# Kernel optimization log

Hardware: AMD Instinct MI355X
Metric: run time of the kernel (lower is better)

## Reference

```python
import jax, jax.numpy as jnp
import numpy as np

N_NODES = 80000
N_EDGES = 1280000
IN_C, HID_C, OUT_C = 128, 64, 40


def setup_inputs() -> dict:
    key = jax.random.key(0)
    k1, k2, k3, k4 = jax.random.split(key, 4)
    x = jax.random.normal(k1, (N_NODES, IN_C), dtype=jnp.float32)
    edge_index = jax.random.randint(k2, (2, N_EDGES), 0, N_NODES, dtype=jnp.int32)
    W1 = jax.random.normal(k3, (IN_C, HID_C), dtype=jnp.float32) * (1.0 / np.sqrt(IN_C))
    W2 = jax.random.normal(k4, (HID_C, OUT_C), dtype=jnp.float32) * (1.0 / np.sqrt(HID_C))
    return {"x": x, "edge_index": edge_index, "W1": W1, "W2": W2}


def _spmm_add(edge_index, h):
    # adj_t.matmul(h): out[dst] += h[src]  (aggr='add', message = x_j)
    src, dst = edge_index[0], edge_index[1]
    return jax.ops.segment_sum(h[src], dst, num_segments=N_NODES)


def reference(x, edge_index, W1, W2):
    # GCNConv 1: linear (no bias) then add-aggregate SpMM
    h = _spmm_add(edge_index, x @ W1)          # [N, HID]
    h = jax.nn.relu(h)
    # GCNConv 2
    h = _spmm_add(edge_index, h @ W2)          # [N, OUT]
    return jax.nn.log_softmax(h, axis=-1)
```

## Files before the change

kernel.cpp:

```cpp
#include <hip/hip_runtime.h>
#include <hip/hip_bf16.h>
#include <math.h>

#define N_NODES 80000
#define N_EDGES 1280000
#define IN_C 128
#define HID_C 64
#define OUT_C 40

#define KB 313
#define BK_CAP 4600
#define EPT_A 8

__device__ __forceinline__ float bf_lo(unsigned u) {
    union { unsigned i; float f; } c; c.i = u << 16; return c.f;
}
__device__ __forceinline__ float bf_hi(unsigned u) {
    union { unsigned i; float f; } c; c.i = u & 0xffff0000u; return c.f;
}
__device__ __forceinline__ unsigned pack_bf2(float a, float b) {
    union { float f; unsigned i; } ca, cb; ca.f = a; cb.f = b;
    unsigned ra = (ca.i + 0x7fffu + ((ca.i >> 16) & 1u)) >> 16;
    unsigned rb = (cb.i + 0x7fffu + ((cb.i >> 16) & 1u)) >> 16;
    return ra | (rb << 16);
}

typedef short v8s __attribute__((ext_vector_type(8)));
typedef float v4f __attribute__((ext_vector_type(4)));
typedef float v2f __attribute__((ext_vector_type(2)));
union U16 { uint4 u; v8s s; };

__device__ __forceinline__ v2f bf2f(unsigned u) {
    return (v2f){bf_lo(u), bf_hi(u)};
}

__global__ void prep_w_kernel(const float* __restrict__ W1, const float* __restrict__ W2,
                              unsigned* __restrict__ w1t, unsigned* __restrict__ w2t,
                              int* __restrict__ bcnt) {
    const int g = blockIdx.x * 256 + threadIdx.x;
    if (g < KB) bcnt[g] = 0;
    {
        const int wcol = g >> 6, kk = g & 63;
        w1t[g] = pack_bf2(W1[(2 * kk) * HID_C + wcol], W1[(2 * kk + 1) * HID_C + wcol]);
    }
    if (g < 1536) {
        const int wcol = g >> 5, kk = g & 31;
        w2t[g] = (wcol < OUT_C)
            ? pack_bf2(W2[(2 * kk) * OUT_C + wcol], W2[(2 * kk + 1) * OUT_C + wcol])
            : 0u;
    }
}

__global__ __launch_bounds__(512) void binA_kernel(const int* __restrict__ src,
                                                   const int* __restrict__ dst,
                                                   int* __restrict__ bcnt,
                                                   int* __restrict__ gbuf) {
    __shared__ int lcnt[KB];
    __shared__ int lexcl[KB];
    __shared__ int lbase[KB];
    __shared__ int lcur[KB];
    __shared__ int stage[512 * EPT_A];
    __shared__ int gaddr[512 * EPT_A];
    const int tid = threadIdx.x;

    for (int i = tid; i < KB; i += 512) lcnt[i] = 0;
    __syncthreads();

    const int e0 = blockIdx.x * 512 * EPT_A;
    int my_s[EPT_A], my_b[EPT_A], my_dl[EPT_A];
#pragma unroll
    for (int j = 0; j < EPT_A; ++j) {
        const int e = e0 + j * 512 + tid;
        if (e < N_EDGES) {
            const int d = dst[e];
            my_s[j] = src[e];
            my_b[j] = d >> 8;
            my_dl[j] = d & 255;
            atomicAdd(&lcnt[my_b[j]], 1);
        } else my_b[j] = -1;
    }
    __syncthreads();

    if (tid < KB) lexcl[tid] = lcnt[tid];
    __syncthreads();
    for (int o = 1; o < KB; o <<= 1) {
        int t = (tid < KB && tid >= o) ? lexcl[tid - o] : 0;
        __syncthreads();
        if (tid < KB) lexcl[tid] += t;
        __syncthreads();
    }
    const int total = lexcl[KB - 1];
    if (tid < KB) {
        lexcl[tid] -= lcnt[tid];
        lbase[tid] = (lcnt[tid] > 0) ? atomicAdd(&bcnt[tid], lcnt[tid]) : 0;
        lcur[tid] = 0;
    }
    __syncthreads();

#pragma unroll
    for (int j = 0; j < EPT_A; ++j) {
        if (my_b[j] >= 0) {
            const int b = my_b[j];
            const int r = atomicAdd(&lcur[b], 1);
            const int li = lexcl[b] + r;
            stage[li] = (my_s[j] << 8) | my_dl[j];
            int gp = lbase[b] + r;
            if (gp >= BK_CAP) gp = BK_CAP - 1;
            gaddr[li] = b * BK_CAP + gp;
        }
    }
    __syncthreads();

    for (int i = tid; i < total; i += 512)
        gbuf[gaddr[i]] = stage[i];
}

__global__ __launch_bounds__(512) void binB_kernel(const int* __restrict__ bcnt,
                                                   const int* __restrict__ gbuf,
                                                   int* __restrict__ rp,
                                                   int* __restrict__ col) {
    __shared__ int sc[KB];
    __shared__ int hist[256];
    __shared__ int excl[256];
    __shared__ int cur[256];
    __shared__ int outb[BK_CAP];
    const int b = blockIdx.x;
    const int tid = threadIdx.x;

    if (tid < KB) sc[tid] = min(bcnt[tid], BK_CAP);
    __syncthreads();
    for (int o = 1; o < KB; o <<= 1) {
        int t = (tid < KB && tid >= o) ? sc[tid - o] : 0;
        __syncthreads();
        if (tid < KB) sc[tid] += t;
        __syncthreads();
    }
    const int n = min(bcnt[b], BK_CAP);
    const int cbase = sc[b] - n;
    const int* __restrict__ my = gbuf + (size_t)b * BK_CAP;

    if (tid < 256) hist[tid] = 0;
    __syncthreads();
    for (int i = tid; i < n; i += 512)
        atomicAdd(&hist[my[i] & 255], 1);
    __syncthreads();

    int h = 0;
    if (tid < 256) { h = hist[tid]; excl[tid] = h; }
    __syncthreads();
    for (int o = 1; o < 256; o <<= 1) {
        int t = (tid < 256 && tid >= o) ? excl[tid - o] : 0;
        __syncthreads();
        if (tid < 256) excl[tid] += t;
        __syncthreads();
    }
    if (tid < 256) {
        const int ex = excl[tid] - h;
        cur[tid] = ex;
        const int node = b * 256 + tid;
        if (node <= N_NODES) rp[node] = cbase + ex;
    }
    __syncthreads();

    for (int i = tid; i < n; i += 512) {
        const int pk = my[i];
        const int pos = atomicAdd(&cur[pk & 255], 1);
        outb[pos] = pk >> 8;
    }
    __syncthreads();
    for (int i = tid; i < n; i += 512)
        col[cbase + i] = outb[i];
}

__global__ __launch_bounds__(256) void gemm1_kernel(const float* __restrict__ x,
                                                    const unsigned* __restrict__ w1t,
                                                    unsigned* __restrict__ h1b) {
    const int wave = threadIdx.x >> 6, lane = threadIdx.x & 63;
    const int nl = lane & 15, quad = lane >> 4;
    const int node = (blockIdx.x * 4 + wave) * 16 + nl;

    v4f acc[4];
#pragma unroll
    for (int q = 0; q < 4; ++q) acc[q] = (v4f){0.f, 0.f, 0.f, 0.f};

#pragma unroll
    for (int kit = 0; kit < 4; ++kit) {
        const float* xp = x + (size_t)node * IN_C + kit * 32 + quad * 8;
        const float4 lo = *(const float4*)xp;
        const float4 hi = *(const float4*)(xp + 4);
        U16 bu;
        bu.u.x = pack_bf2(lo.x, lo.y); bu.u.y = pack_bf2(lo.z, lo.w);
        bu.u.z = pack_bf2(hi.x, hi.y); bu.u.w = pack_bf2(hi.z, hi.w);
#pragma unroll
        for (int mt = 0; mt < 4; ++mt) {
            U16 au;
            au.u = *(const uint4*)(w1t + ((mt * 16 + nl) * 64 + kit * 16 + quad * 4));
            acc[mt] = __builtin_amdgcn_mfma_f32_16x16x32_bf16(au.s, bu.s, acc[mt], 0, 0, 0);
        }
    }
#pragma unroll
    for (int mt = 0; mt < 4; ++mt) {
        uint2 o;
        o.x = pack_bf2(acc[mt][0], acc[mt][1]);
        o.y = pack_bf2(acc[mt][2], acc[mt][3]);
        *(uint2*)(h1b + (size_t)node * 32 + mt * 8 + quad * 2) = o;
    }
}

__global__ void gather64_kernel(const int* __restrict__ rp, const int* __restrict__ col,
                                const unsigned* __restrict__ h1b,
                                unsigned* __restrict__ agg1b) {
    __shared__ int lcol[768];
    const int tid = threadIdx.x;
    const int lane = tid & 63;
    const int wave = tid >> 6;
    const int sl = lane & 31;
    const int es = sl >> 3;
    const int cl = sl & 7;
    const int nb = blockIdx.x * 8;

    const int seg_b = rp[nb];
    const int seg_n = min(rp[nb + 8] - seg_b, 768);
    for (int i = tid; i < seg_n; i += 256) lcol[i] = col[seg_b + i];
    __syncthreads();

    const int node = nb + wave * 2 + (lane >> 5);
    const int b = rp[node], e = rp[node + 1];

    v2f acc[4];
#pragma unroll
    for (int k = 0; k < 4; ++k) acc[k] = (v2f){0.f, 0.f};

    for (int pos = b; __any(pos < e); pos += 32) {
#pragma unroll
        for (int j = 0; j < 8; ++j) {
            const int ei = pos + (j << 2) + es;
            if (ei < e) {
                const int o = ei - seg_b;
                const int s = (o < seg_n) ? lcol[o] : col[ei];
                const uint4 v = *(const uint4*)(h1b + (size_t)s * 32 + cl * 4);
                acc[0] += bf2f(v.x); acc[1] += bf2f(v.y);
                acc[2] += bf2f(v.z); acc[3] += bf2f(v.w);
            }
        }
    }
#pragma unroll
    for (int k = 0; k < 4; ++k) {
        acc[k][0] += __shfl_down(acc[k][0], 16, 64);
        acc[k][1] += __shfl_down(acc[k][1], 16, 64);
    }
#pragma unroll
    for (int k = 0; k < 4; ++k) {
        acc[k][0] += __shfl_down(acc[k][0], 8, 64);
        acc[k][1] += __shfl_down(acc[k][1], 8, 64);
    }

    if (sl < 8) {
        uint4 o;
        o.x = pack_bf2(fmaxf(acc[0][0], 0.f), fmaxf(acc[0][1], 0.f));
        o.y = pack_bf2(fmaxf(acc[1][0], 0.f), fmaxf(acc[1][1], 0.f));
        o.z = pack_bf2(fmaxf(acc[2][0], 0.f), fmaxf(acc[2][1], 0.f));
        o.w = pack_bf2(fmaxf(acc[3][0], 0.f), fmaxf(acc[3][1], 0.f));
        *(uint4*)(agg1b + (size_t)node * 32 + cl * 4) = o;
    }
}

__global__ __launch_bounds__(256) void gemm2_kernel(const unsigned* __restrict__ agg1b,
                                                    const unsigned* __restrict__ w2t,
                                                    unsigned* __restrict__ h2f) {
    const int wave = threadIdx.x >> 6, lane = threadIdx.x & 63;
    const int nl = lane & 15, quad = lane >> 4;
    const int node = (blockIdx.x * 4 + wave) * 16 + nl;

    v4f c[3];
#pragma unroll
    for (int q = 0; q < 3; ++q) c[q] = (v4f){0.f, 0.f, 0.f, 0.f};

#pragma unroll
    for (int kit = 0; kit < 2; ++kit) {
        U16 bu;
        bu.u = *(const uint4*)(agg1b + (size_t)node * 32 + kit * 16 + quad * 4);
#pragma unroll
        for (int mt = 0; mt < 3; ++mt) {
            U16 au;
            au.u = *(const uint4*)(w2t + ((mt * 16 + nl) * 32 + kit * 16 + quad * 4));
            c[mt] = __builtin_amdgcn_mfma_f32_16x16x32_bf16(au.s, bu.s, c[mt], 0, 0, 0);
        }
    }
#pragma unroll
    for (int mt = 0; mt < 3; ++mt) {
        const int idx = mt * 4 + quad;
        if (idx < 10) {
            int u = 0;
            u = __builtin_amdgcn_cvt_pk_fp8_f32(c[mt][0], c[mt][1], u, false);
            u = __builtin_amdgcn_cvt_pk_fp8_f32(c[mt][2], c[mt][3], u, true);
            h2f[(size_t)node * 10 + idx] = (unsigned)u;
        }
    }
}

__global__ void gather40_ls_kernel(const int* __restrict__ rp, const int* __restrict__ col,
                                   const unsigned* __restrict__ h2f,
                                   float* __restrict__ out) {
    __shared__ int lcol[1024];
    const int tid = threadIdx.x;
    const int lane = tid & 63;
    const int wave = tid >> 6;
    const int sl = lane & 15;
    const int es = sl / 5;
    const int cl = sl - es * 5;
    const int gbase = lane & 48;
    const int nb = blockIdx.x * 16;

    const int seg_b = rp[nb];
    const int seg_n = min(rp[nb + 16] - seg_b, 1024);
    for (int i = tid; i < seg_n; i += 256) lcol[i] = col[seg_b + i];
    __syncthreads();

    const int node = nb + wave * 4 + (lane >> 4);
    const int b = rp[node], e = rp[node + 1];

    v2f a[4];
#pragma unroll
    for (int k = 0; k < 4; ++k) a[k] = (v2f){0.f, 0.f};

    for (int pos = b; __any(pos < e); pos += 24) {
#pragma unroll
        for (int j = 0; j < 8; ++j) {
            const int ei = pos + j * 3 + es;
            if ((es < 3) && (ei < e)) {
                const int o = ei - seg_b;
                const int s = (o < seg_n) ? lcol[o] : col[ei];
                const uint2 v = *(const uint2*)(h2f + (size_t)s * 10 + cl * 2);
                a[0] += __builtin_amdgcn_cvt_pk_f32_fp8((int)v.x, false);
                a[1] += __builtin_amdgcn_cvt_pk_f32_fp8((int)v.x, true);
                a[2] += __builtin_amdgcn_cvt_pk_f32_fp8((int)v.y, false);
                a[3] += __builtin_amdgcn_cvt_pk_f32_fp8((int)v.y, true);
            }
        }
    }
#pragma unroll
    for (int k = 0; k < 4; ++k) {
#pragma unroll
        for (int h = 0; h < 2; ++h) {
            const float u = __shfl_down(a[k][h], 5, 64);
            const float w = __shfl_down(a[k][h], 10, 64);
            a[k][h] += u + w;
        }
    }

    const bool own = sl < 5;
    float m = -INFINITY;
    if (own) {
#pragma unroll
        for (int k = 0; k < 4; ++k) m = fmaxf(m, fmaxf(a[k][0], a[k][1]));
    }
    const float m0 = __shfl(m, gbase + 0, 64), m1 = __shfl(m, gbase + 1, 64);
    const float m2 = __shfl(m, gbase + 2, 64), m3 = __shfl(m, gbase + 3, 64);
    const float m4 = __shfl(m, gbase + 4, 64);
    const float gm = fmaxf(fmaxf(fmaxf(m0, m1), fmaxf(m2, m3)), m4);

    float s = 0.f;
    if (own) {
#pragma unroll
        for (int k = 0; k < 4; ++k)
            s += __expf(a[k][0] - gm) + __expf(a[k][1] - gm);
    }
    const float s0 = __shfl(s, gbase + 0, 64), s1 = __shfl(s, gbase + 1, 64);
    const float s2 = __shfl(s, gbase + 2, 64), s3 = __shfl(s, gbase + 3, 64);
    const float s4 = __shfl(s, gbase + 4, 64);
    const float ls = __logf(s0 + s1 + s2 + s3 + s4) + gm;

    if (own) {
        float* op = out + (size_t)node * OUT_C + cl * 8;
        *(float4*)op = make_float4(a[0][0] - ls, a[0][1] - ls, a[1][0] - ls, a[1][1] - ls);
        *(float4*)(op + 4) = make_float4(a[2][0] - ls, a[2][1] - ls, a[3][0] - ls, a[3][1] - ls);
    }
}

extern "C" void kernel_launch(void* const* d_in, const int* in_sizes, int n_in,
                              void* d_out, int out_size, void* d_ws, size_t ws_size,
                              hipStream_t stream) {
    const float* x  = (const float*)d_in[0];
    const int* eidx = (const int*)d_in[1];
    const float* W1 = (const float*)d_in[2];
    const float* W2 = (const float*)d_in[3];
    float* out = (float*)d_out;

    const int* src = eidx;
    const int* dst = eidx + N_EDGES;

    unsigned* h1b   = (unsigned*)d_ws;
    unsigned* agg1b = h1b + (size_t)N_NODES * 32;
    unsigned* h2f   = agg1b + (size_t)N_NODES * 32;
    int*      gbuf  = (int*)(h2f + (size_t)N_NODES * 10);
    int*      col   = gbuf + (size_t)KB * BK_CAP;
    int*      rp    = col + N_EDGES;
    int*      bcnt  = rp + (N_NODES + 1);
    unsigned* w1t   = (unsigned*)(bcnt + KB);
    unsigned* w2t   = w1t + 4096;

    prep_w_kernel<<<16, 256, 0, stream>>>(W1, W2, w1t, w2t, bcnt);
    binA_kernel<<<(N_EDGES + 512 * EPT_A - 1) / (512 * EPT_A), 512, 0, stream>>>(src, dst, bcnt, gbuf);
    binB_kernel<<<KB, 512, 0, stream>>>(bcnt, gbuf, rp, col);
    gemm1_kernel<<<N_NODES / 64, 256, 0, stream>>>(x, w1t, h1b);

    gather64_kernel<<<N_NODES / 8, 256, 0, stream>>>(rp, col, h1b, agg1b);
    gemm2_kernel<<<N_NODES / 64, 256, 0, stream>>>(agg1b, w2t, h2f);
    gather40_ls_kernel<<<N_NODES / 16, 256, 0, stream>>>(rp, col, h2f, out);
}
```

Before: 181.6 us.

## Fuse gemm1 into binning launch and fuse gemm2 into layer-1 gather

The independent dense x@W1 GEMM now runs as extra blocks of the edge-binning kernel, so the two share one launch and can overlap. The second GEMM is fused into the first aggregation kernel: each 512-thread block gathers 16 nodes, stages the ReLU'd bf16 rows in LDS, and one wave computes the 16x40 product with MFMA before writing the fp8 output. This drops the agg1b round trip through global memory and two kernel launches. In exchange, only one of eight waves does the MFMA work after a barrier, and the larger blocks use more LDS, which may lower occupancy in the gather.

```diff
diff --git a/kernel.cpp b/kernel.cpp
--- a/kernel.cpp
+++ b/kernel.cpp
@@ -11,6 +11,8 @@
 #define KB 313
 #define BK_CAP 4600
 #define EPT_A 8
+#define NBLK_A 313
+#define NBLK_G1 625
 
 __device__ __forceinline__ float bf_lo(unsigned u) {
     union { unsigned i; float f; } c; c.i = u << 16; return c.f;
@@ -51,10 +53,48 @@
     }
 }
 
-__global__ __launch_bounds__(512) void binA_kernel(const int* __restrict__ src,
-                                                   const int* __restrict__ dst,
-                                                   int* __restrict__ bcnt,
-                                                   int* __restrict__ gbuf) {
+__global__ __launch_bounds__(512) void binA_gemm1_kernel(const int* __restrict__ src,
+                                                         const int* __restrict__ dst,
+                                                         int* __restrict__ bcnt,
+                                                         int* __restrict__ gbuf,
+                                                         const float* __restrict__ x,
+                                                         const unsigned* __restrict__ w1t,
+                                                         unsigned* __restrict__ h1b) {
+    if (blockIdx.x >= NBLK_A) {
+        const int tid = threadIdx.x;
+        const int wave = tid >> 6, lane = tid & 63;
+        const int nl = lane & 15, quad = lane >> 4;
+        const int node = ((blockIdx.x - NBLK_A) * 8 + wave) * 16 + nl;
+
+        v4f acc[4];
+#pragma unroll
+        for (int q = 0; q < 4; ++q) acc[q] = (v4f){0.f, 0.f, 0.f, 0.f};
+
+#pragma unroll
+        for (int kit = 0; kit < 4; ++kit) {
+            const float* xp = x + (size_t)node * IN_C + kit * 32 + quad * 8;
+            const float4 lo = *(const float4*)xp;
+            const float4 hi = *(const float4*)(xp + 4);
+            U16 bu;
+            bu.u.x = pack_bf2(lo.x, lo.y); bu.u.y = pack_bf2(lo.z, lo.w);
+            bu.u.z = pack_bf2(hi.x, hi.y); bu.u.w = pack_bf2(hi.z, hi.w);
+#pragma unroll
+            for (int mt = 0; mt < 4; ++mt) {
+                U16 au;
+                au.u = *(const uint4*)(w1t + ((mt * 16 + nl) * 64 + kit * 16 + quad * 4));
+                acc[mt] = __builtin_amdgcn_mfma_f32_16x16x32_bf16(au.s, bu.s, acc[mt], 0, 0, 0);
+            }
+        }
+#pragma unroll
+        for (int mt = 0; mt < 4; ++mt) {
+            uint2 o;
+            o.x = pack_bf2(acc[mt][0], acc[mt][1]);
+            o.y = pack_bf2(acc[mt][2], acc[mt][3]);
+            *(uint2*)(h1b + (size_t)node * 32 + mt * 8 + quad * 2) = o;
+        }
+        return;
+    }
+
     __shared__ int lcnt[KB];
     __shared__ int lexcl[KB];
     __shared__ int lbase[KB];
@@ -172,59 +212,28 @@
         col[cbase + i] = outb[i];
 }
 
-__global__ __launch_bounds__(256) void gemm1_kernel(const float* __restrict__ x,
-                                                    const unsigned* __restrict__ w1t,
-                                                    unsigned* __restrict__ h1b) {
-    const int wave = threadIdx.x >> 6, lane = threadIdx.x & 63;
-    const int nl = lane & 15, quad = lane >> 4;
-    const int node = (blockIdx.x * 4 + wave) * 16 + nl;
-
-    v4f acc[4];
-#pragma unroll
-    for (int q = 0; q < 4; ++q) acc[q] = (v4f){0.f, 0.f, 0.f, 0.f};
-
-#pragma unroll
-    for (int kit = 0; kit < 4; ++kit) {
-        const float* xp = x + (size_t)node * IN_C + kit * 32 + quad * 8;
-        const float4 lo = *(const float4*)xp;
-        const float4 hi = *(const float4*)(xp + 4);
-        U16 bu;
-        bu.u.x = pack_bf2(lo.x, lo.y); bu.u.y = pack_bf2(lo.z, lo.w);
-        bu.u.z = pack_bf2(hi.x, hi.y); bu.u.w = pack_bf2(hi.z, hi.w);
-#pragma unroll
-        for (int mt = 0; mt < 4; ++mt) {
-            U16 au;
-            au.u = *(const uint4*)(w1t + ((mt * 16 + nl) * 64 + kit * 16 + quad * 4));
-            acc[mt] = __builtin_amdgcn_mfma_f32_16x16x32_bf16(au.s, bu.s, acc[mt], 0, 0, 0);
-        }
-    }
-#pragma unroll
-    for (int mt = 0; mt < 4; ++mt) {
-        uint2 o;
-        o.x = pack_bf2(acc[mt][0], acc[mt][1]);
-        o.y = pack_bf2(acc[mt][2], acc[mt][3]);
-        *(uint2*)(h1b + (size_t)node * 32 + mt * 8 + quad * 2) = o;
-    }
-}
-
-__global__ void gather64_kernel(const int* __restrict__ rp, const int* __restrict__ col,
-                                const unsigned* __restrict__ h1b,
-                                unsigned* __restrict__ agg1b) {
-    __shared__ int lcol[768];
+__global__ __launch_bounds__(512) void gather64_g2_kernel(const int* __restrict__ rp,
+                                                          const int* __restrict__ col,
+                                                          const unsigned* __restrict__ h1b,
+                                                          const unsigned* __restrict__ w2t,
+                                                          unsigned* __restrict__ h2f) {
+    __shared__ int lcol[1536];
+    __shared__ unsigned aggLds[16 * 36];
     const int tid = threadIdx.x;
     const int lane = tid & 63;
     const int wave = tid >> 6;
     const int sl = lane & 31;
     const int es = sl >> 3;
     const int cl = sl & 7;
-    const int nb = blockIdx.x * 8;
+    const int nb = blockIdx.x * 16;
 
     const int seg_b = rp[nb];
-    const int seg_n = min(rp[nb + 8] - seg_b, 768);
-    for (int i = tid; i < seg_n; i += 256) lcol[i] = col[seg_b + i];
-    __syncthreads();
-
-    const int node = nb + wave * 2 + (lane >> 5);
+    const int seg_n = min(rp[nb + 16] - seg_b, 1536);
+    for (int i = tid; i < seg_n; i += 512) lcol[i] = col[seg_b + i];
+    __syncthreads();
+
+    const int nloc = wave * 2 + (lane >> 5);
+    const int node = nb + nloc;
     const int b = rp[node], e = rp[node + 1];
 
     v2f acc[4];
@@ -261,40 +270,37 @@
         o.y = pack_bf2(fmaxf(acc[1][0], 0.f), fmaxf(acc[1][1], 0.f));
         o.z = pack_bf2(fmaxf(acc[2][0], 0.f), fmaxf(acc[2][1], 0.f));
         o.w = pack_bf2(fmaxf(acc[3][0], 0.f), fmaxf(acc[3][1], 0.f));
-        *(uint4*)(agg1b + (size_t)node * 32 + cl * 4) = o;
-    }
-}
-
-__global__ __launch_bounds__(256) void gemm2_kernel(const unsigned* __restrict__ agg1b,
-                                                    const unsigned* __restrict__ w2t,
-                                                    unsigned* __restrict__ h2f) {
-    const int wave = threadIdx.x >> 6, lane = threadIdx.x & 63;
-    const int nl = lane & 15, quad = lane >> 4;
-    const int node = (blockIdx.x * 4 + wave) * 16 + nl;
-
-    v4f c[3];
-#pragma unroll
-    for (int q = 0; q < 3; ++q) c[q] = (v4f){0.f, 0.f, 0.f, 0.f};
-
-#pragma unroll
-    for (int kit = 0; kit < 2; ++kit) {
-        U16 bu;
-        bu.u = *(const uint4*)(agg1b + (size_t)node * 32 + kit * 16 + quad * 4);
+        *(uint4*)(aggLds + nloc * 36 + cl * 4) = o;
+    }
+    __syncthreads();
+
+    if (wave == 0) {
+        const int nl = lane & 15, quad = lane >> 4;
+        v4f c[3];
+#pragma unroll
+        for (int q = 0; q < 3; ++q) c[q] = (v4f){0.f, 0.f, 0.f, 0.f};
+
+#pragma unroll
+        for (int kit = 0; kit < 2; ++kit) {
+            U16 bu;
+            bu.u = *(const uint4*)(aggLds + nl * 36 + kit * 16 + quad * 4);
+#pragma unroll
+            for (int mt = 0; mt < 3; ++mt) {
+                U16 au;
+                au.u = *(const uint4*)(w2t + ((mt * 16 + nl) * 32 + kit * 16 + quad * 4));
+                c[mt] = __builtin_amdgcn_mfma_f32_16x16x32_bf16(au.s, bu.s, c[mt], 0, 0, 0);
+            }
+        }
+        const int node2 = nb + nl;
 #pragma unroll
         for (int mt = 0; mt < 3; ++mt) {
-            U16 au;
-            au.u = *(const uint4*)(w2t + ((mt * 16 + nl) * 32 + kit * 16 + quad * 4));
-            c[mt] = __builtin_amdgcn_mfma_f32_16x16x32_bf16(au.s, bu.s, c[mt], 0, 0, 0);
-        }
-    }
-#pragma unroll
-    for (int mt = 0; mt < 3; ++mt) {
-        const int idx = mt * 4 + quad;
-        if (idx < 10) {
-            int u = 0;
-            u = __builtin_amdgcn_cvt_pk_fp8_f32(c[mt][0], c[mt][1], u, false);
-            u = __builtin_amdgcn_cvt_pk_fp8_f32(c[mt][2], c[mt][3], u, true);
-            h2f[(size_t)node * 10 + idx] = (unsigned)u;
+            const int idx = mt * 4 + quad;
+            if (idx < 10) {
+                int u = 0;
+                u = __builtin_amdgcn_cvt_pk_fp8_f32(c[mt][0], c[mt][1], u, false);
+                u = __builtin_amdgcn_cvt_pk_fp8_f32(c[mt][2], c[mt][3], u, true);
+                h2f[(size_t)node2 * 10 + idx] = (unsigned)u;
+            }
         }
     }
 }
@@ -401,11 +407,9 @@
     unsigned* w2t   = w1t + 4096;
 
     prep_w_kernel<<<16, 256, 0, stream>>>(W1, W2, w1t, w2t, bcnt);
-    binA_kernel<<<(N_EDGES + 512 * EPT_A - 1) / (512 * EPT_A), 512, 0, stream>>>(src, dst, bcnt, gbuf);
+    binA_gemm1_kernel<<<NBLK_A + NBLK_G1, 512, 0, stream>>>(src, dst, bcnt, gbuf, x, w1t, h1b);
     binB_kernel<<<KB, 512, 0, stream>>>(bcnt, gbuf, rp, col);
-    gemm1_kernel<<<N_NODES / 64, 256, 0, stream>>>(x, w1t, h1b);
-
-    gather64_kernel<<<N_NODES / 8, 256, 0, stream>>>(rp, col, h1b, agg1b);
-    gemm2_kernel<<<N_NODES / 64, 256, 0, stream>>>(agg1b, w2t, h2f);
+
+    gather64_g2_kernel<<<N_NODES / 16, 512, 0, stream>>>(rp, col, h1b, w2t, h2f);
     gather40_ls_kernel<<<N_NODES / 16, 256, 0, stream>>>(rp, col, h2f, out);
 }
```

After: 177.4 us. -2.3%, faster.
